# Kernel tuning notes

Measured on AMD Instinct MI355X. Metric: run time of the kernel, lower is better.

Reference implementation:

```python
import jax, jax.numpy as jnp
import numpy as np

EPS = 1e-08

def squash(x, axis=-1):
    sq = jnp.sum(x * x, axis=axis, keepdims=True)
    scale = sq / (1.0 + sq)
    return scale * x / jnp.sqrt(sq + EPS)

def setup_inputs() -> dict:
    key = jax.random.key(0)
    k1, _ = jax.random.split(key)
    B, IC, OC, D = 128, 1152, 10, 16
    u_predict = jax.random.normal(k1, (B, IC, OC, D), dtype=jnp.float32)
    b = jnp.zeros((IC, OC), dtype=jnp.float32)  # nn.Parameter init
    return {"u_predict": u_predict, "b": b}

def reference(u_predict, b, n_iterations: int = 3):
    # u_predict: (B, IC, OC, D); b: (IC, OC)
    c = jax.nn.softmax(b, axis=1)[None, :, :, None]        # (1, IC, OC, 1)
    s = jnp.sum(c * u_predict, axis=1)                      # (B, OC, D)
    v = squash(s, axis=-1)
    if n_iterations <= 0:
        return v
    b_batch = jnp.broadcast_to(b, u_predict.shape[:3])      # (B, IC, OC)
    for _ in range(n_iterations):
        # agreement: <u_hat, v> over output_dim
        b_batch = b_batch + jnp.einsum('bijd,bjd->bij', u_predict, v)
        c = jax.nn.softmax(b_batch, axis=2)[..., None]      # (B, IC, OC, 1)
        s = jnp.sum(c * u_predict, axis=1)                  # (B, OC, D)
        v = squash(s, axis=-1)
    return v
```

## Files before the change

### kernel.cpp

```cpp
#include <hip/hip_runtime.h>
#include <hip/hip_bf16.h>


#define B_     128
#define IC_    1152
#define OC_    10
#define ROW_   160
#define WPS_   80
#define PARTS_ 8
#define SPB_   144
#define UPB_   9
#define SOUT_  20480

typedef float v2f __attribute__((ext_vector_type(2)));

__device__ __forceinline__ float bf_lo(uint32_t w) { return __uint_as_float(w << 16); }
__device__ __forceinline__ float bf_hi(uint32_t w) { return __uint_as_float(w & 0xffff0000u); }

template<int CTRL>
__device__ __forceinline__ float dppf(float x) {
    return __int_as_float(__builtin_amdgcn_update_dpp(
        0, __float_as_int(x), CTRL, 0xF, 0xF, true));
}
__device__ __forceinline__ float dpp_sum8(float x) {
    x += dppf<0xB1>(x);
    x += dppf<0x4E>(x);
    x += dppf<0x141>(x);
    return x;
}
__device__ __forceinline__ float softmax10(float own[5]) {
    float m = own[0];
#pragma unroll
    for (int k = 1; k < 5; ++k) m = fmaxf(m, own[k]);
    m = fmaxf(m, dppf<0x128>(m));
    float sum = 0.f;
#pragma unroll
    for (int k = 0; k < 5; ++k) { own[k] = __expf(own[k] - m); sum += own[k]; }
    sum += dppf<0x128>(sum);
    return 1.f / sum;
}

__global__ __launch_bounds__(256) void a_kernel(
    const float* __restrict__ u, const float* __restrict__ b_in,
    uint32_t* __restrict__ u16, float* __restrict__ s_part)
{
    const int bid = blockIdx.x, tid = threadIdx.x;
    const int l = tid & 15, h = l >> 3, g = tid >> 4;
    const int b = bid >> 3, part = bid & 7;
    const int wave = tid >> 6, lane = tid & 63;

    __shared__ float red[4][ROW_];
    __shared__ float b_lds[SPB_ * OC_];

#pragma unroll
    for (int it = 0; it < 6; ++it) {
        int idx = it * 256 + tid;
        if (idx < SPB_ * OC_) b_lds[idx] = b_in[part * SPB_ * OC_ + idx];
    }
    __syncthreads();

    float2 sc[5];
#pragma unroll
    for (int k = 0; k < 5; ++k) { sc[k].x = 0.f; sc[k].y = 0.f; }
#pragma unroll
    for (int uu = 0; uu < UPB_; ++uu) {
        const int su = uu * 16 + g;
        const int i  = part * SPB_ + su;
        const v2f* up = (const v2f*)(u + (size_t)(b * IC_ + i) * ROW_ + 2 * l);
        v2f uv[5];
#pragma unroll
        for (int k = 0; k < 5; ++k) uv[k] = __builtin_nontemporal_load(up + 16 * k);

        uint32_t* wp = u16 + (size_t)(b * IC_ + i) * WPS_;
#pragma unroll
        for (int k = 0; k < 5; ++k) {
            __hip_bfloat16 bx = __float2bfloat16(uv[k].x);
            __hip_bfloat16 by = __float2bfloat16(uv[k].y);
            wp[16 * k + l] = ((uint32_t)(*(const uint16_t*)&by) << 16) |
                              (uint32_t)(*(const uint16_t*)&bx);
        }
        float own[5];
#pragma unroll
        for (int k = 0; k < 5; ++k) own[k] = b_lds[su * OC_ + 2 * k + h];
        const float inv = softmax10(own);
#pragma unroll
        for (int k = 0; k < 5; ++k) {
            float c = own[k] * inv;
            sc[k].x += c * uv[k].x; sc[k].y += c * uv[k].y;
        }
    }
#pragma unroll
    for (int k = 0; k < 5; ++k) {
        sc[k].x += __shfl_xor(sc[k].x, 16); sc[k].y += __shfl_xor(sc[k].y, 16);
        sc[k].x += __shfl_xor(sc[k].x, 32); sc[k].y += __shfl_xor(sc[k].y, 32);
    }
    if (lane < 16) {
#pragma unroll
        for (int k = 0; k < 5; ++k)
            *(float2*)&red[wave][32 * k + 2 * l] = sc[k];
    }
    __syncthreads();
    if (tid < ROW_) {
        float t = red[0][tid] + red[1][tid] + red[2][tid] + red[3][tid];
        s_part[(size_t)((0 * B_ + b) * PARTS_ + part) * ROW_ + tid] = t;
    }
}

template<int T>
__global__ __launch_bounds__(256) void i_kernel(
    const uint32_t* __restrict__ u16, const float* __restrict__ b_in,
    const float* __restrict__ s_part, float* __restrict__ s_next)
{
    const int bid = blockIdx.x, tid = threadIdx.x;
    const int l = tid & 15, h = l >> 3, g = tid >> 4;
    const int b = bid >> 3, part = bid & 7;
    const int wave = tid >> 6, lane = tid & 63;

    __shared__ float red[4][ROW_];
    __shared__ float v_lds[ROW_];
    __shared__ float b_lds[SPB_ * OC_];

#pragma unroll
    for (int it = 0; it < 6; ++it) {
        int idx = it * 256 + tid;
        if (idx < SPB_ * OC_) b_lds[idx] = b_in[part * SPB_ * OC_ + idx];
    }

    if (tid < ROW_) {
        float vsum = 0.f;
#pragma unroll
        for (int t = 0; t < T; ++t) {
            const float* sp = s_part + (size_t)((t * B_ + b) * PARTS_) * ROW_;
            float x = 0.f;
#pragma unroll
            for (int p = 0; p < PARTS_; ++p) x += sp[p * ROW_ + tid];
            float sq = x * x;
            sq += __shfl_xor(sq, 1, 16);
            sq += __shfl_xor(sq, 2, 16);
            sq += __shfl_xor(sq, 4, 16);
            sq += __shfl_xor(sq, 8, 16);
            vsum += (sq / (1.f + sq)) * x * rsqrtf(sq + 1e-8f);
        }
        v_lds[tid] = vsum;
    }
    __syncthreads();

    float2 vv[5];
#pragma unroll
    for (int k = 0; k < 5; ++k)
        vv[k] = *(const float2*)&v_lds[32 * k + 2 * l];

    float2 sc[5];
#pragma unroll
    for (int k = 0; k < 5; ++k) { sc[k].x = 0.f; sc[k].y = 0.f; }

#define B_LOAD(UW, uu) do {                                                 \
        const int su_ = (uu) * 16 + g;                                      \
        const uint32_t* wp_ = u16 + (size_t)(b * IC_ + part * SPB_ + su_) * WPS_; \
        _Pragma("unroll")                                                   \
        for (int k = 0; k < 5; ++k) UW[k] = wp_[16 * k + l];                \
    } while (0)

#define B_COMP(UW, uu) do {                                                 \
        const int su_ = (uu) * 16 + g;                                      \
        float own[5];                                                       \
        _Pragma("unroll")                                                   \
        for (int k = 0; k < 5; ++k) own[k] = b_lds[su_ * OC_ + 2 * k + h];  \
        _Pragma("unroll")                                                   \
        for (int k = 0; k < 5; ++k) {                                       \
            float pd = bf_lo(UW[k]) * vv[k].x + bf_hi(UW[k]) * vv[k].y;     \
            own[k] += dpp_sum8(pd);                                         \
        }                                                                   \
        const float inv = softmax10(own);                                   \
        _Pragma("unroll")                                                   \
        for (int k = 0; k < 5; ++k) {                                       \
            float c = own[k] * inv;                                         \
            sc[k].x += c * bf_lo(UW[k]); sc[k].y += c * bf_hi(UW[k]);       \
        }                                                                   \
    } while (0)

    uint32_t uwA[5], uwB[5];
    B_LOAD(uwA, 0);
#pragma clang loop unroll(disable)
    for (int uu = 0; uu < UPB_ - 1; uu += 2) {
        B_LOAD(uwB, uu + 1);
        B_COMP(uwA, uu);
        if (uu + 2 < UPB_) B_LOAD(uwA, uu + 2);
        B_COMP(uwB, uu + 1);
    }
    B_COMP(uwA, UPB_ - 1);
#undef B_LOAD
#undef B_COMP

#pragma unroll
    for (int k = 0; k < 5; ++k) {
        sc[k].x += __shfl_xor(sc[k].x, 16); sc[k].y += __shfl_xor(sc[k].y, 16);
        sc[k].x += __shfl_xor(sc[k].x, 32); sc[k].y += __shfl_xor(sc[k].y, 32);
    }
    if (lane < 16) {
#pragma unroll
        for (int k = 0; k < 5; ++k)
            *(float2*)&red[wave][32 * k + 2 * l] = sc[k];
    }
    __syncthreads();
    if (tid < ROW_) {
        float t = red[0][tid] + red[1][tid] + red[2][tid] + red[3][tid];
        s_next[(size_t)(b * PARTS_ + part) * ROW_ + tid] = t;
    }
}

__global__ __launch_bounds__(256) void f_kernel(
    const float* __restrict__ s_part, float* __restrict__ out)
{
    const int idx = blockIdx.x * 256 + threadIdx.x;
    const int b = idx / ROW_, r = idx % ROW_;
    const float* sp = s_part + (size_t)(b * PARTS_) * ROW_;
    float x = 0.f;
#pragma unroll
    for (int p = 0; p < PARTS_; ++p) x += sp[p * ROW_ + r];
    float sq = x * x;
    sq += __shfl_xor(sq, 1, 16);
    sq += __shfl_xor(sq, 2, 16);
    sq += __shfl_xor(sq, 4, 16);
    sq += __shfl_xor(sq, 8, 16);
    out[idx] = (sq / (1.f + sq)) * x * rsqrtf(sq + 1e-8f);
}

extern "C" void kernel_launch(void* const* d_in, const int* in_sizes, int n_in,
                              void* d_out, int out_size, void* d_ws, size_t ws_size,
                              hipStream_t stream) {
    const float* u    = (const float*)d_in[0];
    const float* b_in = (const float*)d_in[1];
    float* out = (float*)d_out;

    float*    s_part = (float*)d_ws;
    uint32_t* u16    = (uint32_t*)(s_part + 4 * B_ * PARTS_ * ROW_);

    const dim3 blk(256);
    const dim3 grid(B_ * PARTS_);

    a_kernel<<<grid, blk, 0, stream>>>(u, b_in, u16, s_part);
    i_kernel<1><<<grid, blk, 0, stream>>>(u16, b_in, s_part,
                                          s_part + (size_t)1 * B_ * PARTS_ * ROW_);
    i_kernel<2><<<grid, blk, 0, stream>>>(u16, b_in, s_part,
                                          s_part + (size_t)2 * B_ * PARTS_ * ROW_);
    i_kernel<3><<<grid, blk, 0, stream>>>(u16, b_in, s_part,
                                          s_part + (size_t)3 * B_ * PARTS_ * ROW_);
    f_kernel<<<dim3(SOUT_ / 256), blk, 0, stream>>>(
        s_part + (size_t)3 * B_ * PARTS_ * ROW_, out);
}
```

Measured before the change: 71.43 us.

## Reduce partial sums via atomics, carry cumulative v, prefetch u16 early

Iteration kernels now atomically add their per-part sums into a single per-batch s buffer, which a_kernel zeroes. Each iteration reads the previous squashed v sum from a workspace instead of re-reading and re-squashing all earlier partial buffers. This removes the redundant reads of T×8 partials per block and lets the finalize kernel read one value per output. The first two u16 tiles are also prefetched before the b/v setup so load latency overlaps it. The cost is float atomic contention (8 parts per address), non-deterministic summation order, and extra v workspace traffic.

```diff
diff --git a/kernel.cpp b/kernel.cpp
--- a/kernel.cpp
+++ b/kernel.cpp
@@ -39,15 +39,27 @@
     sum += dppf<0x128>(sum);
     return 1.f / sum;
 }
+__device__ __forceinline__ float squash_row(float x) {
+    float sq = x * x;
+    sq += __shfl_xor(sq, 1, 16);
+    sq += __shfl_xor(sq, 2, 16);
+    sq += __shfl_xor(sq, 4, 16);
+    sq += __shfl_xor(sq, 8, 16);
+    return (sq / (1.f + sq)) * x * rsqrtf(sq + 1e-8f);
+}
 
 __global__ __launch_bounds__(256) void a_kernel(
     const float* __restrict__ u, const float* __restrict__ b_in,
-    uint32_t* __restrict__ u16, float* __restrict__ s_part)
+    uint32_t* __restrict__ u16, float* __restrict__ s0_part,
+    float* __restrict__ s_red)
 {
     const int bid = blockIdx.x, tid = threadIdx.x;
     const int l = tid & 15, h = l >> 3, g = tid >> 4;
     const int b = bid >> 3, part = bid & 7;
     const int wave = tid >> 6, lane = tid & 63;
+
+    const int gidx = bid * 256 + tid;
+    if (gidx < 3 * SOUT_) s_red[gidx] = 0.f;
 
     __shared__ float red[4][ROW_];
     __shared__ float b_lds[SPB_ * OC_];
@@ -102,14 +114,16 @@
     __syncthreads();
     if (tid < ROW_) {
         float t = red[0][tid] + red[1][tid] + red[2][tid] + red[3][tid];
-        s_part[(size_t)((0 * B_ + b) * PARTS_ + part) * ROW_ + tid] = t;
+        s0_part[(size_t)(b * PARTS_ + part) * ROW_ + tid] = t;
     }
 }
 
 template<int T>
 __global__ __launch_bounds__(256) void i_kernel(
     const uint32_t* __restrict__ u16, const float* __restrict__ b_in,
-    const float* __restrict__ s_part, float* __restrict__ s_next)
+    const float* __restrict__ s0_part, const float* __restrict__ s_red_prev,
+    const float* __restrict__ v_in, float* __restrict__ v_out,
+    float* __restrict__ s_out)
 {
     const int bid = blockIdx.x, tid = threadIdx.x;
     const int l = tid & 15, h = l >> 3, g = tid >> 4;
@@ -120,6 +134,17 @@
     __shared__ float v_lds[ROW_];
     __shared__ float b_lds[SPB_ * OC_];
 
+#define B_LOAD(UW, uu) do {                                                 \
+        const int su_ = (uu) * 16 + g;                                      \
+        const uint32_t* wp_ = u16 + (size_t)(b * IC_ + part * SPB_ + su_) * WPS_; \
+        _Pragma("unroll")                                                   \
+        for (int k = 0; k < 5; ++k) UW[k] = wp_[16 * k + l];                \
+    } while (0)
+
+    uint32_t uwA[5], uwB[5];
+    B_LOAD(uwA, 0);
+    B_LOAD(uwB, 1);
+
 #pragma unroll
     for (int it = 0; it < 6; ++it) {
         int idx = it * 256 + tid;
@@ -127,20 +152,17 @@
     }
 
     if (tid < ROW_) {
-        float vsum = 0.f;
-#pragma unroll
-        for (int t = 0; t < T; ++t) {
-            const float* sp = s_part + (size_t)((t * B_ + b) * PARTS_) * ROW_;
+        float vsum;
+        if (T == 1) {
+            const float* sp = s0_part + (size_t)(b * PARTS_) * ROW_;
             float x = 0.f;
 #pragma unroll
             for (int p = 0; p < PARTS_; ++p) x += sp[p * ROW_ + tid];
-            float sq = x * x;
-            sq += __shfl_xor(sq, 1, 16);
-            sq += __shfl_xor(sq, 2, 16);
-            sq += __shfl_xor(sq, 4, 16);
-            sq += __shfl_xor(sq, 8, 16);
-            vsum += (sq / (1.f + sq)) * x * rsqrtf(sq + 1e-8f);
+            vsum = squash_row(x);
+        } else {
+            vsum = v_in[b * ROW_ + tid] + squash_row(s_red_prev[b * ROW_ + tid]);
         }
+        if (T < 3 && part == 0) v_out[b * ROW_ + tid] = vsum;
         v_lds[tid] = vsum;
     }
     __syncthreads();
@@ -153,13 +175,6 @@
     float2 sc[5];
 #pragma unroll
     for (int k = 0; k < 5; ++k) { sc[k].x = 0.f; sc[k].y = 0.f; }
-
-#define B_LOAD(UW, uu) do {                                                 \
-        const int su_ = (uu) * 16 + g;                                      \
-        const uint32_t* wp_ = u16 + (size_t)(b * IC_ + part * SPB_ + su_) * WPS_; \
-        _Pragma("unroll")                                                   \
-        for (int k = 0; k < 5; ++k) UW[k] = wp_[16 * k + l];                \
-    } while (0)
 
 #define B_COMP(UW, uu) do {                                                 \
         const int su_ = (uu) * 16 + g;                                      \
@@ -179,14 +194,12 @@
         }                                                                   \
     } while (0)
 
-    uint32_t uwA[5], uwB[5];
-    B_LOAD(uwA, 0);
 #pragma clang loop unroll(disable)
     for (int uu = 0; uu < UPB_ - 1; uu += 2) {
-        B_LOAD(uwB, uu + 1);
         B_COMP(uwA, uu);
         if (uu + 2 < UPB_) B_LOAD(uwA, uu + 2);
         B_COMP(uwB, uu + 1);
+        if (uu + 3 < UPB_) B_LOAD(uwB, uu + 3);
     }
     B_COMP(uwA, UPB_ - 1);
 #undef B_LOAD
@@ -205,25 +218,15 @@
     __syncthreads();
     if (tid < ROW_) {
         float t = red[0][tid] + red[1][tid] + red[2][tid] + red[3][tid];
-        s_next[(size_t)(b * PARTS_ + part) * ROW_ + tid] = t;
+        atomicAdd(&s_out[b * ROW_ + tid], t);
     }
 }
 
 __global__ __launch_bounds__(256) void f_kernel(
-    const float* __restrict__ s_part, float* __restrict__ out)
+    const float* __restrict__ s3, float* __restrict__ out)
 {
     const int idx = blockIdx.x * 256 + threadIdx.x;
-    const int b = idx / ROW_, r = idx % ROW_;
-    const float* sp = s_part + (size_t)(b * PARTS_) * ROW_;
-    float x = 0.f;
-#pragma unroll
-    for (int p = 0; p < PARTS_; ++p) x += sp[p * ROW_ + r];
-    float sq = x * x;
-    sq += __shfl_xor(sq, 1, 16);
-    sq += __shfl_xor(sq, 2, 16);
-    sq += __shfl_xor(sq, 4, 16);
-    sq += __shfl_xor(sq, 8, 16);
-    out[idx] = (sq / (1.f + sq)) * x * rsqrtf(sq + 1e-8f);
+    out[idx] = squash_row(s3[idx]);
 }
 
 extern "C" void kernel_launch(void* const* d_in, const int* in_sizes, int n_in,
@@ -233,19 +236,20 @@
     const float* b_in = (const float*)d_in[1];
     float* out = (float*)d_out;
 
-    float*    s_part = (float*)d_ws;
-    uint32_t* u16    = (uint32_t*)(s_part + 4 * B_ * PARTS_ * ROW_);
+    float*    s0_part = (float*)d_ws;
+    float*    s_red   = s0_part + (size_t)B_ * PARTS_ * ROW_;
+    float*    v_acc   = s_red + 3 * SOUT_;
+    uint32_t* u16     = (uint32_t*)(v_acc + 2 * SOUT_);
 
     const dim3 blk(256);
     const dim3 grid(B_ * PARTS_);
 
-    a_kernel<<<grid, blk, 0, stream>>>(u, b_in, u16, s_part);
-    i_kernel<1><<<grid, blk, 0, stream>>>(u16, b_in, s_part,
-                                          s_part + (size_t)1 * B_ * PARTS_ * ROW_);
-    i_kernel<2><<<grid, blk, 0, stream>>>(u16, b_in, s_part,
-                                          s_part + (size_t)2 * B_ * PARTS_ * ROW_);
-    i_kernel<3><<<grid, blk, 0, stream>>>(u16, b_in, s_part,
-                                          s_part + (size_t)3 * B_ * PARTS_ * ROW_);
-    f_kernel<<<dim3(SOUT_ / 256), blk, 0, stream>>>(
-        s_part + (size_t)3 * B_ * PARTS_ * ROW_, out);
-}
+    a_kernel<<<grid, blk, 0, stream>>>(u, b_in, u16, s0_part, s_red);
+    i_kernel<1><<<grid, blk, 0, stream>>>(u16, b_in, s0_part, nullptr,
+                                          nullptr, v_acc, s_red);
+    i_kernel<2><<<grid, blk, 0, stream>>>(u16, b_in, s0_part, s_red,
+                                          v_acc, v_acc + SOUT_, s_red + SOUT_);
+    i_kernel<3><<<grid, blk, 0, stream>>>(u16, b_in, s0_part, s_red + SOUT_,
+                                          v_acc + SOUT_, nullptr, s_red + 2 * SOUT_);
+    f_kernel<<<dim3(SOUT_ / 256), blk, 0, stream>>>(s_red + 2 * SOUT_, out);
+}
```

Measured after the change: 68.88 us. 1.04x faster.
